# Optimization experiments

Measured on AMD Instinct MI355X. Metric: run time of the kernel, lower is better.

Reference implementation:

```python
import jax, jax.numpy as jnp
import numpy as np

B, D, H, E, C = 8192, 1024, 4096, 8, 1024


def setup_inputs() -> dict:
    key = jax.random.key(0)
    ks = jax.random.split(key, 7)
    s_d = 1.0 / np.sqrt(D)
    s_h = 1.0 / np.sqrt(H)
    return {
        "x": jax.random.normal(ks[0], (B, D), dtype=jnp.float32),
        "W1": jax.random.normal(ks[1], (E, D, H), dtype=jnp.float32) * s_d,  # fc1 per expert
        "b1": jnp.zeros((E, H), dtype=jnp.float32),
        "W2": jax.random.normal(ks[2], (E, H, C), dtype=jnp.float32) * s_h,  # fc2 per expert
        "b2": jnp.zeros((E, C), dtype=jnp.float32),
        "Wg": jax.random.normal(ks[3], (D, E), dtype=jnp.float32) * s_d,     # gating fc
        "bg": jnp.zeros((E,), dtype=jnp.float32),
    }


def reference(x, W1, b1, W2, b2, Wg, bg):
    # gating: softmax over experts
    gating_weights = jax.nn.softmax(x @ Wg + bg, axis=1)            # [B, E]
    # dense MoE: every expert on every token, batched over E
    h = jax.nn.relu(jnp.einsum('bd,edh->beh', x, W1) + b1)          # [B, E, H]
    expert_outputs = jnp.einsum('beh,ehc->bec', h, W2) + b2         # [B, E, C]
    mixture_output = jnp.einsum('be,bec->bc', gating_weights, expert_outputs)  # [B, C]
    return (mixture_output, gating_weights, expert_outputs)
```

## Files before the change

kernel.cpp:

```cpp
#include <hip/hip_runtime.h>

#define B_TOK 8192
#define D_DIM 1024
#define H_DIM 4096
#define E_NUM 8
#define C_DIM 1024

typedef unsigned short ushort_t;
typedef __attribute__((ext_vector_type(8))) short bf16x8;
typedef __attribute__((ext_vector_type(4))) float f32x4;

__device__ inline ushort_t f2bf(float f) {
    unsigned u = __float_as_uint(f);
    unsigned r = (u + 0x7fffu + ((u >> 16) & 1u)) >> 16;
    return (ushort_t)r;
}

__device__ inline void async16(const ushort_t* g, void* l) {
    __builtin_amdgcn_global_load_lds((__attribute__((address_space(1))) void*)g,
                                     (__attribute__((address_space(3))) void*)l,
                                     16, 0, 0);
}

template <bool FC1>
__global__ __launch_bounds__(256) void gemm_bt(
    const ushort_t* __restrict__ A, const ushort_t* __restrict__ Bt,
    const float* __restrict__ bias, ushort_t* __restrict__ outH,
    float* __restrict__ outF, int M, int N, int K, int ldc)
{
    __shared__ __align__(16) ushort_t As[128 * 32];
    __shared__ __align__(16) ushort_t Bs[128 * 32];

    const int tid  = threadIdx.x;
    const int w    = tid >> 6;
    const int lane = tid & 63;
    const int wm   = w >> 1, wn = w & 1;
    const int m0 = blockIdx.y * 128, n0 = blockIdx.x * 128;

    const int o1 = w * 2048 + lane * 16;
    const int o2 = o1 + 1024;
    const int r1 = o1 >> 6;
    const int kk = (o1 & 63) >> 1;

    const ushort_t* pa = A  + (size_t)(m0 + r1) * K + kk;
    const ushort_t* pb = Bt + (size_t)(n0 + r1) * K + kk;
    const size_t rowstep = (size_t)16 * K;

    char* ldsA1 = (char*)As + o1; char* ldsA2 = (char*)As + o2;
    char* ldsB1 = (char*)Bs + o1; char* ldsB2 = (char*)Bs + o2;

    f32x4 acc[4][4];
#pragma unroll
    for (int i = 0; i < 4; i++)
#pragma unroll
        for (int j = 0; j < 4; j++) acc[i][j] = (f32x4){0.f, 0.f, 0.f, 0.f};

    const bf16x8* Asv = (const bf16x8*)As;
    const bf16x8* Bsv = (const bf16x8*)Bs;
    const int ar = (wm * 64 + (lane & 15)) * 4 + (lane >> 4);
    const int br = (wn * 64 + (lane & 15)) * 4 + (lane >> 4);

    for (int kt = 0; kt < K; kt += 32) {
        async16(pa, ldsA1);
        async16(pa + rowstep, ldsA2);
        async16(pb, ldsB1);
        async16(pb + rowstep, ldsB2);
        pa += 32; pb += 32;
        __syncthreads();

        bf16x8 af[4], bg_[4];
#pragma unroll
        for (int i = 0; i < 4; i++) af[i] = Asv[ar + i * 64];
#pragma unroll
        for (int j = 0; j < 4; j++) bg_[j] = Bsv[br + j * 64];
#pragma unroll
        for (int i = 0; i < 4; i++)
#pragma unroll
            for (int j = 0; j < 4; j++)
                acc[i][j] = __builtin_amdgcn_mfma_f32_16x16x32_bf16(
                    af[i], bg_[j], acc[i][j], 0, 0, 0);
        __syncthreads();
    }

    const int colq = lane & 15, rowq = (lane >> 4) * 4;
#pragma unroll
    for (int j = 0; j < 4; j++) {
        int col = n0 + wn * 64 + j * 16 + colq;
        float bv = bias[col];
#pragma unroll
        for (int i = 0; i < 4; i++) {
            int rowb = m0 + wm * 64 + i * 16 + rowq;
#pragma unroll
            for (int r = 0; r < 4; r++) {
                float v = acc[i][j][r] + bv;
                if (FC1) {
                    v = v > 0.f ? v : 0.f;
                    outH[(size_t)(rowb + r) * ldc + col] = f2bf(v);
                } else {
                    outF[(size_t)(rowb + r) * ldc + col] = v;
                }
            }
        }
    }
}

__global__ __launch_bounds__(256) void transpose_cvt(
    const float* __restrict__ in, ushort_t* __restrict__ out, int R, int C)
{
    __shared__ float t[32][33];
    int c0 = blockIdx.x * 32, r0 = blockIdx.y * 32;
    int tx = threadIdx.x, ty = threadIdx.y;
#pragma unroll
    for (int i = 0; i < 4; i++)
        t[ty + i * 8][tx] = in[(size_t)(r0 + ty + i * 8) * C + c0 + tx];
    __syncthreads();
#pragma unroll
    for (int i = 0; i < 4; i++)
        out[(size_t)(c0 + ty + i * 8) * R + r0 + tx] = f2bf(t[tx][ty + i * 8]);
}

__global__ __launch_bounds__(256) void cvt_bf16x4(
    const float* __restrict__ in, ushort_t* __restrict__ out)
{
    int i = blockIdx.x * 256 + threadIdx.x;
    float4 v = ((const float4*)in)[i];
    unsigned lo = (unsigned)f2bf(v.x) | ((unsigned)f2bf(v.y) << 16);
    unsigned hi = (unsigned)f2bf(v.z) | ((unsigned)f2bf(v.w) << 16);
    ((uint2*)out)[i] = make_uint2(lo, hi);
}

__global__ __launch_bounds__(256) void gating_kernel(
    const float* __restrict__ x, const float* __restrict__ Wg,
    const float* __restrict__ bg, float* __restrict__ gw)
{
    int lane = threadIdx.x & 63;
    int b = blockIdx.x * 4 + (threadIdx.x >> 6);
    const float* xr = x + (size_t)b * D_DIM;
    float acc[8] = {0, 0, 0, 0, 0, 0, 0, 0};
    for (int k = 0; k < D_DIM / 64; k++) {
        int d = k * 64 + lane;
        float xv = xr[d];
        const float4* wr = (const float4*)(Wg + (size_t)d * 8);
        float4 w0 = wr[0], w1 = wr[1];
        acc[0] += xv * w0.x; acc[1] += xv * w0.y;
        acc[2] += xv * w0.z; acc[3] += xv * w0.w;
        acc[4] += xv * w1.x; acc[5] += xv * w1.y;
        acc[6] += xv * w1.z; acc[7] += xv * w1.w;
    }
#pragma unroll
    for (int off = 32; off > 0; off >>= 1)
#pragma unroll
        for (int e = 0; e < 8; e++) acc[e] += __shfl_xor(acc[e], off, 64);

    float mx = -1e30f;
#pragma unroll
    for (int e = 0; e < 8; e++) { acc[e] += bg[e]; mx = fmaxf(mx, acc[e]); }
    float s = 0.f;
#pragma unroll
    for (int e = 0; e < 8; e++) { acc[e] = expf(acc[e] - mx); s += acc[e]; }
    float outv = acc[0];
#pragma unroll
    for (int e = 1; e < 8; e++) outv = (lane == e) ? acc[e] : outv;
    if (lane < 8) gw[(size_t)b * 8 + lane] = outv / s;
}

__global__ __launch_bounds__(256) void mixture_kernel(
    const float* __restrict__ gw, const float* __restrict__ eo,
    float* __restrict__ mix)
{
    int b = blockIdx.x, t = threadIdx.x;
    float g[8];
#pragma unroll
    for (int e = 0; e < 8; e++) g[e] = gw[(size_t)b * 8 + e];
    const float4* ep = (const float4*)(eo + (size_t)b * (E_NUM * C_DIM));
    float4 a = make_float4(0.f, 0.f, 0.f, 0.f);
#pragma unroll
    for (int e = 0; e < 8; e++) {
        float4 v = ep[e * 256 + t];
        a.x += g[e] * v.x; a.y += g[e] * v.y;
        a.z += g[e] * v.z; a.w += g[e] * v.w;
    }
    ((float4*)(mix + (size_t)b * C_DIM))[t] = a;
}

extern "C" void kernel_launch(void* const* d_in, const int* in_sizes, int n_in,
                              void* d_out, int out_size, void* d_ws,
                              size_t ws_size, hipStream_t stream)
{
    const float* x  = (const float*)d_in[0];
    const float* W1 = (const float*)d_in[1];
    const float* b1 = (const float*)d_in[2];
    const float* W2 = (const float*)d_in[3];
    const float* b2 = (const float*)d_in[4];
    const float* Wg = (const float*)d_in[5];
    const float* bg = (const float*)d_in[6];

    float* mix = (float*)d_out;
    float* gw  = mix + (size_t)B_TOK * C_DIM;
    float* eo  = gw + (size_t)B_TOK * E_NUM;

    ushort_t* xb  = (ushort_t*)d_ws;
    ushort_t* w1t = xb + (size_t)B_TOK * D_DIM;
    ushort_t* w2t = w1t + (size_t)H_DIM * D_DIM;
    ushort_t* hb  = w2t + (size_t)C_DIM * H_DIM;

    cvt_bf16x4<<<(B_TOK * D_DIM) / 1024, 256, 0, stream>>>(x, xb);
    gating_kernel<<<B_TOK / 4, 256, 0, stream>>>(x, Wg, bg, gw);

    for (int e = 0; e < E_NUM; e++) {
        transpose_cvt<<<dim3(H_DIM / 32, D_DIM / 32), dim3(32, 8), 0, stream>>>(
            W1 + (size_t)e * D_DIM * H_DIM, w1t, D_DIM, H_DIM);
        gemm_bt<true><<<dim3(H_DIM / 128, B_TOK / 128), 256, 0, stream>>>(
            xb, w1t, b1 + (size_t)e * H_DIM, hb, nullptr,
            B_TOK, H_DIM, D_DIM, H_DIM);
        transpose_cvt<<<dim3(C_DIM / 32, H_DIM / 32), dim3(32, 8), 0, stream>>>(
            W2 + (size_t)e * H_DIM * C_DIM, w2t, H_DIM, C_DIM);
        gemm_bt<false><<<dim3(C_DIM / 128, B_TOK / 128), 256, 0, stream>>>(
            hb, w2t, b2 + (size_t)e * C_DIM, nullptr, eo + (size_t)e * C_DIM,
            B_TOK, C_DIM, H_DIM, E_NUM * C_DIM);
    }

    mixture_kernel<<<B_TOK, 256, 0, stream>>>(gw, eo, mix);
}
```

Measured before the change: 2.145 ms.

## Add double-buffered 256x256 pipelined GEMM kernel for FC1

Replaces the FC1 GEMM (128x128 tile, single LDS buffer, two barriers per 32-wide k step) with a 256x256-tile, 512-thread kernel. It double-buffers 64-wide K slices in LDS, uses XOR-swizzled LDS layouts to avoid bank conflicts, and interleaves async global-to-LDS loads with MFMA quarters using setprio and manual waitcnt. The goal is to hide memory latency and raise MFMA utilisation for the dominant GEMM. In exchange it uses much more LDS (128KB per block), relies on hand-tuned waitcnt ordering, and wraps prefetch offsets modulo K, so it issues redundant loads at the tail.

```diff
diff --git a/kernel.cpp b/kernel.cpp
--- a/kernel.cpp
+++ b/kernel.cpp
@@ -20,6 +20,158 @@
     __builtin_amdgcn_global_load_lds((__attribute__((address_space(1))) void*)g,
                                      (__attribute__((address_space(3))) void*)l,
                                      16, 0, 0);
+}
+
+#define FENCE() asm volatile("" ::: "memory")
+#define BARRIER() do { FENCE(); __builtin_amdgcn_s_barrier(); FENCE(); } while (0)
+#define WAITLGKM0() asm volatile("s_waitcnt lgkmcnt(0)" ::: "memory")
+#define WAITVM4()   asm volatile("s_waitcnt vmcnt(4)" ::: "memory")
+
+
+#define MFMAQ(AF, BF, mq, nq)                                                  \
+  _Pragma("unroll") for (int mi = 0; mi < 4; mi++)                             \
+  _Pragma("unroll") for (int ni = 0; ni < 2; ni++)                             \
+  _Pragma("unroll") for (int kc = 0; kc < 2; kc++)                             \
+    acc[(mq) * 4 + mi][(nq) * 2 + ni] =                                        \
+        __builtin_amdgcn_mfma_f32_16x16x32_bf16(                               \
+            AF[mi][kc], BF[ni][kc], acc[(mq) * 4 + mi][(nq) * 2 + ni], 0, 0, 0);
+
+#define GROUP(AVc, BVc, stA, stB, ktc)                                         \
+  {                                                                            \
+    int kA = (ktc) + 64;  if (kA >= K) kA -= K;                                \
+    int kB = (ktc) + 128; if (kB >= K) kB -= K;                                \
+    const ushort_t* gA = pa + kA;                                              \
+    const ushort_t* gB = pb + kB;                                              \
+                                                        \
+    _Pragma("unroll") for (int mi = 0; mi < 4; mi++)                           \
+      _Pragma("unroll") for (int kc = 0; kc < 2; kc++)                         \
+        af[mi][kc] = (AVc)[aBase + (mi * 16) * 8 + ck[kc]];                    \
+    _Pragma("unroll") for (int ni = 0; ni < 2; ni++)                           \
+      _Pragma("unroll") for (int kc = 0; kc < 2; kc++)                         \
+        bq0[ni][kc] = (BVc)[bBase + (ni * 16) * 8 + ck[kc]];                   \
+    async16(gA,       (stA));                                                  \
+    async16(gA + R64, (stA) + 8192);                                           \
+    BARRIER(); WAITLGKM0();                                                    \
+    __builtin_amdgcn_s_setprio(1);                                             \
+    MFMAQ(af, bq0, 0, 0);                                                      \
+    __builtin_amdgcn_s_setprio(0);                                             \
+    BARRIER();                                                                 \
+                                                        \
+    _Pragma("unroll") for (int ni = 0; ni < 2; ni++)                           \
+      _Pragma("unroll") for (int kc = 0; kc < 2; kc++)                         \
+        bq1[ni][kc] = (BVc)[bBase + (32 + ni * 16) * 8 + ck[kc]];              \
+    async16(gA + R128,       (stA) + 16384);                                   \
+    async16(gA + R128 + R64, (stA) + 16384 + 8192);                            \
+    BARRIER(); WAITLGKM0();                                                    \
+    __builtin_amdgcn_s_setprio(1);                                             \
+    MFMAQ(af, bq1, 0, 1);                                                      \
+    __builtin_amdgcn_s_setprio(0);                                             \
+    BARRIER();                                                                 \
+                                                        \
+    _Pragma("unroll") for (int mi = 0; mi < 4; mi++)                           \
+      _Pragma("unroll") for (int kc = 0; kc < 2; kc++)                         \
+        af[mi][kc] = (AVc)[aBase + (64 + mi * 16) * 8 + ck[kc]];               \
+    async16(gB,       (stB));                                                  \
+    async16(gB + R64, (stB) + 8192);                                           \
+    BARRIER(); WAITLGKM0();                                                    \
+    __builtin_amdgcn_s_setprio(1);                                             \
+    MFMAQ(af, bq1, 1, 1);                                                      \
+    __builtin_amdgcn_s_setprio(0);                                             \
+    BARRIER();                                                                 \
+                                                        \
+    async16(gB + R128,       (stB) + 16384);                                   \
+    async16(gB + R128 + R64, (stB) + 16384 + 8192);                            \
+    BARRIER();                                                                 \
+    __builtin_amdgcn_s_setprio(1);                                             \
+    MFMAQ(af, bq0, 1, 0);                                                      \
+    __builtin_amdgcn_s_setprio(0);                                             \
+    WAITVM4();                                                                 \
+    BARRIER();                                                                 \
+  }
+
+__global__ __launch_bounds__(512, 2) void gemm256_fc1(
+    const ushort_t* __restrict__ A, const ushort_t* __restrict__ Bt,
+    const float* __restrict__ bias, ushort_t* __restrict__ outH,
+    int M, int N, int K, int ldc)
+{
+    __shared__ __align__(16) ushort_t As[2][256 * 64];
+    __shared__ __align__(16) ushort_t Bs[2][256 * 64];
+
+    const int tid  = threadIdx.x;
+    const int lane = tid & 63;
+    const int w    = tid >> 6;
+    const int wm   = w >> 2, wn = w & 3;
+    const int m0 = blockIdx.y * 256, n0 = blockIdx.x * 256;
+
+    const int l15 = lane & 15, l4 = lane >> 4, l7 = lane & 7;
+
+    const int srow   = tid >> 3;
+    const int schunk = (tid & 7) ^ (srow & 7);
+    const size_t R64  = (size_t)64 * K;
+    const size_t R128 = (size_t)128 * K;
+    const ushort_t* pa = A  + (size_t)(m0 + srow) * K + schunk * 8;
+    const ushort_t* pb = Bt + (size_t)(n0 + srow) * K + schunk * 8;
+    char* const stA0 = (char*)&As[0][0] + tid * 16;
+    char* const stA1 = (char*)&As[1][0] + tid * 16;
+    char* const stB0 = (char*)&Bs[0][0] + tid * 16;
+    char* const stB1 = (char*)&Bs[1][0] + tid * 16;
+
+    const bf16x8* Av0 = (const bf16x8*)&As[0][0];
+    const bf16x8* Av1 = (const bf16x8*)&As[1][0];
+    const bf16x8* Bv0 = (const bf16x8*)&Bs[0][0];
+    const bf16x8* Bv1 = (const bf16x8*)&Bs[1][0];
+    const int aBase = (wm * 128 + l15) * 8;
+    const int bBase = (wn * 64 + l15) * 8;
+    const int ck[2] = { l4 ^ l7, (4 + l4) ^ l7 };
+
+    f32x4 acc[8][4];
+#pragma unroll
+    for (int i = 0; i < 8; i++)
+#pragma unroll
+        for (int j = 0; j < 4; j++) acc[i][j] = (f32x4){0.f, 0.f, 0.f, 0.f};
+
+    bf16x8 af[4][2], bq0[2][2], bq1[2][2];
+
+    async16(pa,              stA0);
+    async16(pa + R64,        stA0 + 8192);
+    async16(pa + R128,       stA0 + 16384);
+    async16(pa + R128 + R64, stA0 + 16384 + 8192);
+    async16(pb,              stB0);
+    async16(pb + R64,        stB0 + 8192);
+    async16(pb + R128,       stB0 + 16384);
+    async16(pb + R128 + R64, stB0 + 16384 + 8192);
+    async16(pb + 64,              stB1);
+    async16(pb + 64 + R64,        stB1 + 8192);
+    async16(pb + 64 + R128,       stB1 + 16384);
+    async16(pb + 64 + R128 + R64, stB1 + 16384 + 8192);
+    WAITVM4();
+    BARRIER();
+
+    for (int kt = 0; kt < K; kt += 128) {
+        GROUP(Av0, Bv0, stA1, stB0, kt);
+        GROUP(Av1, Bv1, stA0, stB1, kt + 64);
+    }
+
+    const int colq = l15, rowq = l4 * 4;
+#pragma unroll
+    for (int nq = 0; nq < 2; nq++)
+#pragma unroll
+    for (int ni = 0; ni < 2; ni++) {
+        int col = n0 + wn * 64 + nq * 32 + ni * 16 + colq;
+        float bv = bias[col];
+#pragma unroll
+        for (int mq = 0; mq < 2; mq++)
+#pragma unroll
+        for (int mi = 0; mi < 4; mi++) {
+            int rowb = m0 + wm * 128 + mq * 64 + mi * 16 + rowq;
+#pragma unroll
+            for (int r = 0; r < 4; r++) {
+                float v = acc[mq * 4 + mi][nq * 2 + ni][r] + bv;
+                v = v > 0.f ? v : 0.f;
+                outH[(size_t)(rowb + r) * ldc + col] = f2bf(v);
+            }
+        }
+    }
 }
 
 template <bool FC1>
@@ -210,9 +362,8 @@
     for (int e = 0; e < E_NUM; e++) {
         transpose_cvt<<<dim3(H_DIM / 32, D_DIM / 32), dim3(32, 8), 0, stream>>>(
             W1 + (size_t)e * D_DIM * H_DIM, w1t, D_DIM, H_DIM);
-        gemm_bt<true><<<dim3(H_DIM / 128, B_TOK / 128), 256, 0, stream>>>(
-            xb, w1t, b1 + (size_t)e * H_DIM, hb, nullptr,
-            B_TOK, H_DIM, D_DIM, H_DIM);
+        gemm256_fc1<<<dim3(H_DIM / 256, B_TOK / 256), 512, 0, stream>>>(
+            xb, w1t, b1 + (size_t)e * H_DIM, hb, B_TOK, H_DIM, D_DIM, H_DIM);
         transpose_cvt<<<dim3(C_DIM / 32, H_DIM / 32), dim3(32, 8), 0, stream>>>(
             W2 + (size_t)e * H_DIM * C_DIM, w2t, H_DIM, C_DIM);
         gemm_bt<false><<<dim3(C_DIM / 128, B_TOK / 128), 256, 0, stream>>>(
```

Result: faster. 2.086 ms (-2.8%).
